# Performance work log

Hardware: AMD Instinct MI355X
Metric: run time of the kernel (lower is better)

Reference implementation:

```python
import jax, jax.numpy as jnp
import numpy as np

EPS = 1e-12  # clamp before sqrt, matching torch cdist-style euclidean_dist stability


def euclidean_dist(x, y):
    # x: (N, D), y: (M, D) -> (N, M)
    x2 = jnp.sum(x * x, axis=-1, keepdims=True)          # (N, 1)
    y2 = jnp.sum(y * y, axis=-1)                          # (M,)
    d2 = x2 + y2 - 2.0 * (x @ y.T)
    return jnp.sqrt(jnp.clip(d2, EPS))


def setup_inputs() -> dict:
    key = jax.random.key(0)
    k1, k2 = jax.random.split(key)
    B, W, H, D, M = 8, 28, 28, 128, 16384
    embedding = jax.random.normal(k1, (B * W * H, D), dtype=jnp.float32)
    memory_bank = jax.random.normal(k2, (M, D), dtype=jnp.float32)
    return {"embedding": embedding, "memory_bank": memory_bank,
            "batch_size": B, "width": W, "height": H}


def reference(embedding, memory_bank, batch_size, width, height):
    num_neighbors = 9
    B = batch_size
    D = embedding.shape[-1]
    Mb = memory_bank.shape[0]

    # get_nearest_neighbors with num_neighbors=1 (topk smallest)
    dist = euclidean_dist(embedding, memory_bank)                 # (N, M) -- dominant cost
    neg_vals, locations = jax.lax.top_k(-dist, 1)                 # smallest-1
    patch_scores = (-neg_vals).reshape(B, -1)                     # (B, P)
    locations = locations.reshape(B, -1)                          # (B, P)

    # compute_anomaly_score (num_neighbors > 1 branch)
    b = jnp.arange(B)
    max_patches = jnp.argmax(patch_scores, axis=1)                # (B,)
    emb3 = embedding.reshape(B, -1, D)
    max_patches_features = emb3[b, max_patches]                   # (B, D)
    score = patch_scores[b, max_patches]                          # (B,)
    nn_index = locations[b, max_patches]                          # (B,)
    nn_sample = memory_bank[nn_index]                             # (B, D)

    k = min(num_neighbors, Mb)
    d_nn = euclidean_dist(nn_sample, memory_bank)                 # (B, M)
    _, support_samples = jax.lax.top_k(-d_nn, k)                  # (B, k) smallest-k
    support_feats = memory_bank[support_samples]                  # (B, k, D)

    # batched euclidean dist: (B,1,D) vs (B,k,D) -> (B,k)
    x = max_patches_features[:, None, :]
    d2 = (jnp.sum(x * x, -1) + jnp.sum(support_feats * support_feats, -1)
          - 2.0 * jnp.einsum('bid,bkd->bk', x, support_feats))
    distances = jnp.sqrt(jnp.clip(d2, EPS))                       # (B, k)

    weights = (1.0 - jax.nn.softmax(distances, axis=1))[:, 0]     # (B,)
    return weights * score
```

## Files before the change

### kernel.cpp

```cpp
#include <hip/hip_runtime.h>
#include <cstdint>

#define N_EMB 6272
#define DIMD  128
#define M_BANK 16384
#define BATCH 8
#define PPB   784
#define KNN   9
#define EPSF  1e-12f
#define NKB   64

typedef unsigned long long u64;
typedef _Float16 f16x8 __attribute__((ext_vector_type(8)));
typedef _Float16 f16x2 __attribute__((ext_vector_type(2)));
typedef float    f32x4 __attribute__((ext_vector_type(4)));

static __device__ __forceinline__ u64 umin64(u64 a, u64 b) { return b < a ? b : a; }
static __device__ __forceinline__ u64 umax64(u64 a, u64 b) { return b > a ? b : a; }

static __device__ __forceinline__ void gll16(const _Float16* g, _Float16* l) {
    __builtin_amdgcn_global_load_lds(
        (__attribute__((address_space(1))) void*)(const void*)g,
        (__attribute__((address_space(3))) void*)l, 16, 0, 0);
}

static __device__ __forceinline__ float dot8(f16x8 a, f16x8 b, float c) {
#if __has_builtin(__builtin_amdgcn_fdot2)
    const f16x2* pa = (const f16x2*)&a;
    const f16x2* pb = (const f16x2*)&b;
    c = __builtin_amdgcn_fdot2(pa[0], pb[0], c, false);
    c = __builtin_amdgcn_fdot2(pa[1], pb[1], c, false);
    c = __builtin_amdgcn_fdot2(pa[2], pb[2], c, false);
    c = __builtin_amdgcn_fdot2(pa[3], pb[3], c, false);
#else
    #pragma unroll
    for (int e = 0; e < 8; ++e) c += (float)a[e] * (float)b[e];
#endif
    return c;
}

__global__ __launch_bounds__(256) void convert_kernel(
        const float* __restrict__ emb, const float* __restrict__ bank,
        _Float16* __restrict__ GAh, _Float16* __restrict__ GBh,
        float* __restrict__ x2, float* __restrict__ y2,
        unsigned* __restrict__ packed32, u64* __restrict__ binfo) {
    const int gid = blockIdx.x * 256 + threadIdx.x;
    if (gid < N_EMB) packed32[gid] = 0x7f800000u;
    if (gid < BATCH) binfo[gid] = ~0ull;
    const int row = gid >> 4;
    const int chunk = gid & 15;
    const float* src;
    _Float16* dh;
    float* nrm;
    int R;
    if (row < M_BANK) {
        src = bank + (size_t)row * DIMD; dh = GBh; nrm = y2; R = row;
    } else {
        R = row - M_BANK;
        src = emb + (size_t)R * DIMD; dh = GAh; nrm = x2;
    }
    float4 v0 = ((const float4*)src)[chunk * 2];
    float4 v1 = ((const float4*)src)[chunk * 2 + 1];
    float f[8] = {v0.x, v0.y, v0.z, v0.w, v1.x, v1.y, v1.z, v1.w};
    f16x8 h;
    float s = 0.f;
    #pragma unroll
    for (int e = 0; e < 8; ++e) {
        h[e] = (_Float16)f[e];
        s += f[e] * f[e];
    }
    const int q = chunk >> 2, jj = chunk & 3;
    const int jj2 = jj ^ ((R >> 1) & 3);
    *(f16x8*)(dh + (size_t)R * DIMD + q * 32 + jj2 * 8) = h;
    #pragma unroll
    for (int off = 1; off < 16; off <<= 1) s += __shfl_xor(s, off, 16);
    if (chunk == 0) nrm[R] = s;
}


static __device__ __forceinline__ void stageB(
        const _Float16* __restrict__ GBh, _Float16* dst,
        int mrow0, int h, int srow, int se8) {
    #pragma unroll
    for (int j = 0; j < 2; ++j) {
        const int row = srow + j * 64;
        #pragma unroll
        for (int q = 0; q < 2; ++q)
            gll16(GBh + (size_t)(mrow0 + row) * DIMD + h * 64 + q * 32 + se8,
                  dst + q * 4096 + row * 32 + se8);
    }
}

template<int H, bool FIRST>
static __device__ __forceinline__ void computeB(
        const _Float16* bb, const f16x8 (&a)[4][4], f32x4 (&acc)[4][4],
        int wm, int g, int r16) {
    f16x8 b[4][2];
    #pragma unroll
    for (int fj = 0; fj < 4; ++fj) {
        const int row = wm * 64 + fj * 16 + r16;
        const int sw = (g ^ ((row >> 1) & 3)) << 3;
        b[fj][0] = *(const f16x8*)&bb[row * 32 + sw];
        b[fj][1] = *(const f16x8*)&bb[4096 + row * 32 + sw];
    }
    const f32x4 zero = {0.f, 0.f, 0.f, 0.f};
    #pragma unroll
    for (int ks = 0; ks < 2; ++ks)
        #pragma unroll
        for (int fi = 0; fi < 4; ++fi)
            #pragma unroll
            for (int fj = 0; fj < 4; ++fj)
                acc[fi][fj] = __builtin_amdgcn_mfma_f32_16x16x32_f16(
                    a[fi][2 * H + ks], b[fj][ks],
                    (FIRST && ks == 0) ? zero : acc[fi][fj], 0, 0, 0);
}

__global__ __launch_bounds__(256, 2) void dist_min_mfma(
        const _Float16* __restrict__ GAh, const _Float16* __restrict__ GBh,
        const float* __restrict__ x2, const float* __restrict__ y2,
        unsigned* __restrict__ packed32) {
    __shared__ _Float16 smem[16384];

    const int bid = blockIdx.x;
    const int c   = bid & 15;
    const int nt  = bid >> 4;
    const int n0  = nt * 128;
    const int mbase = c * 1024;

    const int tid  = threadIdx.x;
    const int lane = tid & 63;
    const int wid  = tid >> 6;
    const int wn = wid >> 1, wm = wid & 1;
    const int g = lane >> 4, r16 = lane & 15;
    const int srow = tid >> 2;
    const int se8  = (tid & 3) * 8;

    _Float16* sB0 = smem;
    _Float16* sB1 = smem + 8192;

    f16x8 a[4][4];
    #pragma unroll
    for (int h = 0; h < 2; ++h) {
        #pragma unroll
        for (int k = 0; k < 2; ++k)
            #pragma unroll
            for (int j = 0; j < 2; ++j) {
                const int row = srow + j * 64;
                gll16(GAh + (size_t)(n0 + row) * DIMD + (h * 2 + k) * 32 + se8,
                      smem + k * 4096 + row * 32 + se8);
            }
        __syncthreads();
        #pragma unroll
        for (int fi = 0; fi < 4; ++fi) {
            const int row = wn * 64 + fi * 16 + r16;
            const int sw = (g ^ ((row >> 1) & 3)) << 3;
            #pragma unroll
            for (int k = 0; k < 2; ++k)
                a[fi][h * 2 + k] = *(const f16x8*)&smem[k * 4096 + row * 32 + sw];
        }
        __syncthreads();
    }

    stageB(GBh, sB0, mbase, 0, srow, se8);
    __syncthreads();

    f32x4 acc[4][4];
    float runmin[4][4];
    #pragma unroll
    for (int fi = 0; fi < 4; ++fi)
        #pragma unroll
        for (int r = 0; r < 4; ++r) runmin[fi][r] = 3.4e38f;

    for (int t = 0; t < 8; ++t) {
        const int mt = mbase + t * 128;
        stageB(GBh, sB1, mt, 1, srow, se8);
        computeB<0, true>(sB0, a, acc, wm, g, r16);
        __syncthreads();
        if (t < 7) stageB(GBh, sB0, mt + 128, 0, srow, se8);
        float ys[4];
        #pragma unroll
        for (int fj = 0; fj < 4; ++fj)
            ys[fj] = y2[mt + wm * 64 + fj * 16 + r16];
        computeB<1, false>(sB1, a, acc, wm, g, r16);

        #pragma unroll
        for (int fi = 0; fi < 4; ++fi)
            #pragma unroll
            for (int r = 0; r < 4; ++r) {
                float d0 = fmaf(-2.f, acc[fi][0][r], ys[0]);
                float d1 = fmaf(-2.f, acc[fi][1][r], ys[1]);
                float d2v = fmaf(-2.f, acc[fi][2][r], ys[2]);
                float d3 = fmaf(-2.f, acc[fi][3][r], ys[3]);
                runmin[fi][r] = fminf(runmin[fi][r],
                                      fminf(fminf(d0, d1), fminf(d2v, d3)));
            }
        __syncthreads();
    }

    #pragma unroll
    for (int fi = 0; fi < 4; ++fi) {
        #pragma unroll
        for (int r = 0; r < 4; ++r) {
            const int n = n0 + wn * 64 + fi * 16 + g * 4 + r;
            float v = runmin[fi][r];
            #pragma unroll
            for (int off = 1; off < 16; off <<= 1)
                v = fminf(v, __shfl_xor(v, off));
            if (r16 == 0) {
                float d2 = fmaxf(x2[n] + v, EPSF);
                atomicMin(&packed32[n], __float_as_uint(d2));
            }
        }
    }
}

__global__ __launch_bounds__(256) void nn_find(
        const unsigned* __restrict__ packed32,
        const _Float16* __restrict__ GAh, const _Float16* __restrict__ GBh,
        const float* __restrict__ x2, const float* __restrict__ y2,
        u64* __restrict__ binfo, unsigned* __restrict__ pstar) {
    const int b = blockIdx.y, tid = threadIdx.x;
    __shared__ u64 red[256];
    __shared__ unsigned s_p;
    __shared__ _Float16 xv[DIMD];

    u64 bk = 0;
    for (int p = tid; p < PPB; p += 256) {
        unsigned bits = packed32[(size_t)b * PPB + p];
        bk = umax64(bk, ((u64)bits << 32) | (u64)(0xFFFFFFFFu - (unsigned)p));
    }
    red[tid] = bk; __syncthreads();
    for (int s = 128; s; s >>= 1) {
        if (tid < s) red[tid] = umax64(red[tid], red[tid + s]);
        __syncthreads();
    }
    if (tid == 0) s_p = 0xFFFFFFFFu - (unsigned)red[0];
    __syncthreads();
    const unsigned p = s_p;
    if (blockIdx.x == 0 && tid == 0) pstar[b] = p;

    const int Ra = b * PPB + (int)p;
    if (tid < DIMD) xv[tid] = GAh[(size_t)Ra * DIMD + tid];
    const float xr2 = x2[Ra];
    __syncthreads();

    const int m = blockIdx.x * 256 + tid;
    const int delta = (((Ra >> 1) ^ (m >> 1)) & 3);
    const _Float16* row = GBh + (size_t)m * DIMD;
    float dot = 0.f;
    #pragma unroll
    for (int q = 0; q < 4; ++q)
        #pragma unroll
        for (int jj2 = 0; jj2 < 4; ++jj2) {
            f16x8 ym = *(const f16x8*)(row + q * 32 + jj2 * 8);
            f16x8 xm = *(const f16x8*)&xv[q * 32 + (jj2 ^ delta) * 8];
            dot = dot8(ym, xm, dot);
        }
    float d2 = fmaxf(xr2 + y2[m] - 2.0f * dot, EPSF);
    u64 key = ((u64)__float_as_uint(d2) << 32) | (unsigned)m;
    red[tid] = key; __syncthreads();
    for (int s = 128; s; s >>= 1) {
        if (tid < s) red[tid] = umin64(red[tid], red[tid + s]);
        __syncthreads();
    }
    if (tid == 0) atomicMin(&binfo[b], red[0]);
}

__global__ __launch_bounds__(256) void knn_kernel(
        const u64* __restrict__ binfo,
        const _Float16* __restrict__ GBh,
        const float* __restrict__ y2,
        u64* __restrict__ cand) {
    const int b = blockIdx.y, tid = threadIdx.x;
    __shared__ u64 red4[4];
    __shared__ u64 s_wkey;
    __shared__ _Float16 nv[DIMD];

    const unsigned nn = (unsigned)binfo[b];
    if (tid < DIMD) nv[tid] = GBh[(size_t)nn * DIMD + tid];
    __syncthreads();

    const int m = blockIdx.x * 256 + tid;
    const int delta = (((nn >> 1) ^ (m >> 1)) & 3);
    const _Float16* row = GBh + (size_t)m * DIMD;
    float dot = 0.f;
    #pragma unroll
    for (int q = 0; q < 4; ++q)
        #pragma unroll
        for (int jj2 = 0; jj2 < 4; ++jj2) {
            f16x8 ym = *(const f16x8*)(row + q * 32 + jj2 * 8);
            f16x8 xm = *(const f16x8*)&nv[q * 32 + (jj2 ^ delta) * 8];
            dot = dot8(ym, xm, dot);
        }
    float d2 = fmaxf(y2[nn] + y2[m] - 2.0f * dot, EPSF);
    const u64 mykey = ((u64)__float_as_uint(d2) << 32) | (unsigned)m;

    u64* myout = cand + ((size_t)b * NKB + blockIdx.x) * KNN;
    bool used = false;
    for (int r = 0; r < KNN; ++r) {
        u64 h = used ? ~0ull : mykey;
        #pragma unroll
        for (int off = 1; off < 64; off <<= 1)
            h = umin64(h, (u64)__shfl_xor((unsigned long long)h, off));
        if ((tid & 63) == 0) red4[tid >> 6] = h;
        __syncthreads();
        if (tid == 0) {
            u64 w = umin64(umin64(red4[0], red4[1]), umin64(red4[2], red4[3]));
            s_wkey = w;
            myout[r] = w;
        }
        __syncthreads();
        if (!used && mykey == s_wkey) used = true;
    }
}

__global__ __launch_bounds__(256) void final_kernel(
        const float* __restrict__ emb, const float* __restrict__ bank,
        const float* __restrict__ x2, const float* __restrict__ y2,
        const u64* __restrict__ binfo, const unsigned* __restrict__ pstar,
        const u64* __restrict__ cand,
        float* __restrict__ out) {
    const int b = blockIdx.x, tid = threadIdx.x;
    __shared__ u64 lists[256 * 3];
    __shared__ float fred[256];
    __shared__ u64 red4[4];
    __shared__ u64 s_wkey;
    __shared__ unsigned s_sel[KNN];
    __shared__ float s_dist[KNN];
    __shared__ float xv[DIMD];

    const unsigned p = pstar[b];
    const unsigned nn = (unsigned)binfo[b];

    float prod = 0.f;
    if (tid < DIMD) {
        float xvv = emb[(size_t)(b * PPB + p) * DIMD + tid];
        xv[tid] = xvv;
        prod = xvv * bank[(size_t)nn * DIMD + tid];
    }
    fred[tid] = prod; __syncthreads();
    for (int s = 128; s; s >>= 1) {
        if (tid < s) fred[tid] += fred[tid + s];
        __syncthreads();
    }
    const float d2star = fmaxf(x2[b * PPB + p] + y2[nn] - 2.0f * fred[0], EPSF);

    u64 lst[3] = {~0ull, ~0ull, ~0ull};
    #pragma unroll
    for (int i = 0; i < 3; ++i) {
        const int idx = tid * 3 + i;
        if (idx < NKB * KNN) {
            u64 k = cand[(size_t)b * NKB * KNN + idx];
            lst[2] = k;
            u64 a0 = lst[0], a1 = lst[1], a2 = lst[2];
            u64 t01l = umin64(a0, a1), t01h = umax64(a0, a1);
            u64 m2 = umin64(t01h, a2), h2 = umax64(t01h, a2);
            lst[0] = umin64(t01l, m2);
            lst[1] = umax64(t01l, m2);
            lst[2] = h2;
        }
    }
    lists[tid * 3 + 0] = lst[0];
    lists[tid * 3 + 1] = lst[1];
    lists[tid * 3 + 2] = lst[2];
    __syncthreads();

    int pp = 0;
    for (int r = 0; r < KNN; ++r) {
        u64 h = (pp < 3) ? lists[tid * 3 + pp] : ~0ull;
        #pragma unroll
        for (int off = 1; off < 64; off <<= 1)
            h = umin64(h, (u64)__shfl_xor((unsigned long long)h, off));
        if ((tid & 63) == 0) red4[tid >> 6] = h;
        __syncthreads();
        if (tid == 0) {
            u64 w = umin64(umin64(red4[0], red4[1]), umin64(red4[2], red4[3]));
            s_wkey = w;
            s_sel[r] = (unsigned)w;
        }
        __syncthreads();
        const u64 w = s_wkey;
        if (pp < 3 && lists[tid * 3 + pp] == w) ++pp;
    }

    if (tid < KNN) {
        const unsigned s = s_sel[tid];
        const float* srow = bank + (size_t)s * DIMD;
        float dot = 0.f;
        for (int d = 0; d < DIMD; ++d) dot += srow[d] * xv[d];
        float d2 = x2[b * PPB + p] + y2[s] - 2.0f * dot;
        s_dist[tid] = sqrtf(fmaxf(d2, EPSF));
    }
    __syncthreads();

    if (tid == 0) {
        float mx = s_dist[0];
        for (int i = 1; i < KNN; ++i) mx = fmaxf(mx, s_dist[i]);
        float sum = 0.f, e0 = 0.f;
        for (int i = 0; i < KNN; ++i) {
            float e = expf(s_dist[i] - mx);
            sum += e;
            if (i == 0) e0 = e;
        }
        float w = 1.0f - e0 / sum;
        out[b] = w * sqrtf(d2star);
    }
}

extern "C" void kernel_launch(void* const* d_in, const int* in_sizes, int n_in,
                              void* d_out, int out_size, void* d_ws, size_t ws_size,
                              hipStream_t stream) {
    const float* emb  = (const float*)d_in[0];
    const float* bank = (const float*)d_in[1];
    float* out = (float*)d_out;

    char* ws = (char*)d_ws;
    unsigned* packed32 = (unsigned*) (ws + 0);
    float*    x2       = (float*)    (ws + 32768);
    float*    y2       = (float*)    (ws + 65536);
    u64*      binfo    = (u64*)      (ws + 131072);
    unsigned* pstar    = (unsigned*) (ws + 131200);
    u64*      cand     = (u64*)      (ws + 135168);
    _Float16* GAh      = (_Float16*) (ws + 262144);
    _Float16* GBh      = (_Float16*) (ws + 1867776);

    {
        const int rows = M_BANK + N_EMB;
        const int blocks = rows * 16 / 256;
        convert_kernel<<<blocks, 256, 0, stream>>>(emb, bank, GAh, GBh, x2, y2,
                                                   packed32, binfo);
    }

    dist_min_mfma<<<49 * 16, 256, 0, stream>>>(GAh, GBh, x2, y2, packed32);

    nn_find<<<dim3(NKB, BATCH), 256, 0, stream>>>(packed32, GAh, GBh, x2, y2,
                                                  binfo, pstar);

    knn_kernel<<<dim3(NKB, BATCH), 256, 0, stream>>>(binfo, GBh, y2, cand);

    final_kernel<<<BATCH, 256, 0, stream>>>(emb, bank, x2, y2, binfo, pstar,
                                            cand, out);
}
```

Before: 80.04 us.

## Prefetch y2 into LDS and replace syncthreads with fine-grained vmcnt barriers

Loads the block's 1024 y2 norms into shared memory once at kernel start through global_load_lds, so the per-tile global y2 reads go away. The __syncthreads calls in the main loop become raw s_barrier plus explicit s_waitcnt vmcnt(4) and sched_barrier, letting the next B-tile load stay in flight while the current tile is computed. The risk is a correctness dependence on hand-counted outstanding loads and on barrier placement, which must match what stageB actually issues.

```diff
diff --git a/kernel.cpp b/kernel.cpp
--- a/kernel.cpp
+++ b/kernel.cpp
@@ -119,7 +119,8 @@
         const _Float16* __restrict__ GAh, const _Float16* __restrict__ GBh,
         const float* __restrict__ x2, const float* __restrict__ y2,
         unsigned* __restrict__ packed32) {
-    __shared__ _Float16 smem[16384];
+    __shared__ _Float16 smem[18432];
+    float* sY = (float*)(smem + 16384);
 
     const int bid = blockIdx.x;
     const int c   = bid & 15;
@@ -138,6 +139,8 @@
     _Float16* sB0 = smem;
     _Float16* sB1 = smem + 8192;
 
+    gll16((const _Float16*)(y2 + mbase) + (size_t)tid * 8, smem + 16384 + tid * 8);
+
     f16x8 a[4][4];
     #pragma unroll
     for (int h = 0; h < 2; ++h) {
@@ -162,7 +165,6 @@
     }
 
     stageB(GBh, sB0, mbase, 0, srow, se8);
-    __syncthreads();
 
     f32x4 acc[4][4];
     float runmin[4][4];
@@ -173,28 +175,39 @@
 
     for (int t = 0; t < 8; ++t) {
         const int mt = mbase + t * 128;
+        __builtin_amdgcn_s_barrier();
+        __builtin_amdgcn_sched_barrier(0);
         stageB(GBh, sB1, mt, 1, srow, se8);
+        asm volatile("s_waitcnt vmcnt(4)" ::: "memory");
+        __builtin_amdgcn_s_barrier();
+        __builtin_amdgcn_sched_barrier(0);
         computeB<0, true>(sB0, a, acc, wm, g, r16);
-        __syncthreads();
-        if (t < 7) stageB(GBh, sB0, mt + 128, 0, srow, se8);
-        float ys[4];
-        #pragma unroll
-        for (int fj = 0; fj < 4; ++fj)
-            ys[fj] = y2[mt + wm * 64 + fj * 16 + r16];
+        __builtin_amdgcn_s_barrier();
+        __builtin_amdgcn_sched_barrier(0);
+        if (t < 7) {
+            stageB(GBh, sB0, mt + 128, 0, srow, se8);
+            asm volatile("s_waitcnt vmcnt(4)" ::: "memory");
+        } else {
+            asm volatile("s_waitcnt vmcnt(0)" ::: "memory");
+        }
+        __builtin_amdgcn_s_barrier();
+        __builtin_amdgcn_sched_barrier(0);
         computeB<1, false>(sB1, a, acc, wm, g, r16);
 
+        const int tofs = t * 128 + wm * 64 + r16;
+        const float ys0 = sY[tofs +  0], ys1 = sY[tofs + 16];
+        const float ys2 = sY[tofs + 32], ys3 = sY[tofs + 48];
         #pragma unroll
         for (int fi = 0; fi < 4; ++fi)
             #pragma unroll
             for (int r = 0; r < 4; ++r) {
-                float d0 = fmaf(-2.f, acc[fi][0][r], ys[0]);
-                float d1 = fmaf(-2.f, acc[fi][1][r], ys[1]);
-                float d2v = fmaf(-2.f, acc[fi][2][r], ys[2]);
-                float d3 = fmaf(-2.f, acc[fi][3][r], ys[3]);
+                float d0 = fmaf(-2.f, acc[fi][0][r], ys0);
+                float d1 = fmaf(-2.f, acc[fi][1][r], ys1);
+                float d2v = fmaf(-2.f, acc[fi][2][r], ys2);
+                float d3 = fmaf(-2.f, acc[fi][3][r], ys3);
                 runmin[fi][r] = fminf(runmin[fi][r],
                                       fminf(fminf(d0, d1), fminf(d2v, d3)));
             }
-        __syncthreads();
     }
 
     #pragma unroll
```

Result: no change. 79.96 us (median of 2 runs) (-0.1%).
